# Optimization experiments

Hardware: AMD Instinct MI355X
Metric: run time of the kernel (lower is better)

The kernel has to match this reference:

```python
import jax, jax.numpy as jnp
import numpy as np

B, C, N, M = 4, 192, 160, 160
HEADS, DH = 4, 32
HID = HEADS * DH
NMEM = 4
SCALE = DH ** -0.5


def setup_inputs() -> dict:
    key = jax.random.key(0)
    ks = jax.random.split(key, 8)
    std = 0.05
    return {
        "x": jax.random.normal(ks[0], (B, C, N, M), jnp.float32),
        "gq": jnp.ones((C,), jnp.float32),
        "gk": jnp.ones((C,), jnp.float32),
        "gv": jnp.ones((C,), jnp.float32),
        "Wq": jax.random.normal(ks[1], (HID, C), jnp.float32) * std,
        "Wk": jax.random.normal(ks[2], (HID, C), jnp.float32) * std,
        "Wv": jax.random.normal(ks[3], (HID, C), jnp.float32) * std,
        "mem_kv": jax.random.normal(ks[4], (2, HEADS, NMEM, DH), jnp.float32),
        "Wo": jax.random.normal(ks[5], (C, HID), jnp.float32) * std,
        "bo": jnp.zeros((C,), jnp.float32),
        "Wr": jax.random.normal(ks[6], (C, 2 * C), jnp.float32) * std,
    }


def _rms(x, g):
    # lucidrains RMSNorm over channel axis 1: F.normalize(x, dim=1) * g * sqrt(dim)
    n = jnp.sqrt(jnp.sum(x * x, axis=1, keepdims=True))
    gshape = (1, -1) + (1,) * (x.ndim - 2)
    return x / jnp.maximum(n, 1e-12) * g.reshape(gshape) * jnp.sqrt(jnp.asarray(x.shape[1], x.dtype))


def _axial_attn(q_ft, k_ft, v_map, rep, Wq, Wk, Wv, mem_kv, Wo, bo, gq, gk, gv):
    # q_ft: (b, c, Lq) compact queries (spatial (1,Lq) in the original)
    # k_ft: (b, c, Lk) compact keys; original repeats them `rep` times -> (Lk*rep) keys
    # v_map: (b, c, Lk, rep) values (full map, not broadcast)
    # Exact math of softmax over [NMEM + Lk*rep] keys, exploiting the rep-fold
    # duplicated key scores so attn(key i, copy j) has identical weight p_i:
    #   out = sum_mem p_j mem_v_j + sum_i p_i * (sum_rep v[i, r])
    b = q_ft.shape[0]
    q = jnp.einsum('hdc,bcq->bhqd', Wq.reshape(HEADS, DH, -1), _rms(q_ft, gq))
    k = jnp.einsum('hdc,bck->bhkd', Wk.reshape(HEADS, DH, -1), _rms(k_ft, gk))
    v = jnp.einsum('hdc,bckr->bhkrd', Wv.reshape(HEADS, DH, -1), _rms(v_map, gv))
    v_sum = v.sum(axis=3)  # (b,h,Lk,d)
    mem_k, mem_v = mem_kv[0], mem_kv[1]
    s_k = jnp.einsum('bhqd,bhkd->bhqk', q, k) * SCALE      # (b,h,Lq,Lk)
    s_m = jnp.einsum('bhqd,hjd->bhqj', q, mem_k) * SCALE   # (b,h,Lq,NMEM)
    mx = jnp.maximum(s_k.max(-1), s_m.max(-1))             # (b,h,Lq)
    e_k = jnp.exp(s_k - mx[..., None])
    e_m = jnp.exp(s_m - mx[..., None])
    Z = e_m.sum(-1) + rep * e_k.sum(-1)                    # rep copies of each key
    out = (jnp.einsum('bhqj,hjd->bhqd', e_m, mem_v)
           + jnp.einsum('bhqk,bhkd->bhqd', e_k, v_sum)) / Z[..., None]
    out = out.transpose(0, 2, 1, 3).reshape(b, -1, HID)    # (b,Lq,hid), (h d) channel order
    return jnp.einsum('ck,bqk->bcq', Wo, out) + bo[None, :, None]  # (b,c,Lq)


def reference(x, gq, gk, gv, Wq, Wk, Wv, mem_kv, Wo, bo, Wr):
    # x: (b,c,n,m); mask=None path
    row_ft = x.mean(axis=3)  # (b,c,n)
    col_ft = x.mean(axis=2)  # (b,c,m)
    # row attention: n queries, keys = col_ft repeated n times, values = x^T (spatial (m,n))
    row_attn = _axial_attn(row_ft, col_ft, x.transpose(0, 1, 3, 2), N,
                           Wq, Wk, Wv, mem_kv, Wo, bo, gq, gk, gv)  # (b,c,n)
    # col attention (shared weights): m queries, keys = row_ft repeated m times, values = x
    col_attn = _axial_attn(col_ft, row_ft, x, M,
                           Wq, Wk, Wv, mem_kv, Wo, bo, gq, gk, gv)  # (b,c,m)
    # broadcast to (b,c,n,m), concat on channels, 1x1 conv reduce (bias=False)
    Wr1, Wr2 = Wr[:, :C], Wr[:, C:]
    out = (jnp.einsum('dc,bcn->bdn', Wr1, row_attn)[:, :, :, None]
           + jnp.einsum('dc,bcm->bdm', Wr2, col_attn)[:, :, None, :])
    return out
```

## Files before the change

### kernel.cpp

```cpp
#include <hip/hip_runtime.h>
#include <math.h>

constexpr int B_ = 4, C_ = 192, N_ = 160, M_ = 160;
constexpr int NM_ = N_ * M_;
constexpr float SQRT_C = 13.856406460551018f;
constexpr float SCALE_ = 0.17677669529663687f;

__device__ __forceinline__ float wred_sum(float v) {
    #pragma unroll
    for (int o = 32; o > 0; o >>= 1) v += __shfl_xor(v, o, 64);
    return v;
}
__device__ __forceinline__ float wred_max(float v) {
    #pragma unroll
    for (int o = 32; o > 0; o >>= 1) v = fmaxf(v, __shfl_xor(v, o, 64));
    return v;
}

__global__ __launch_bounds__(256) void prep_rn_kernel(
        const float* __restrict__ x,
        const float* __restrict__ Wr, const float* __restrict__ Wo,
        const float* __restrict__ bo,
        const float* __restrict__ Wq, const float* __restrict__ Wk,
        const float* __restrict__ Wv, const float* __restrict__ gq,
        const float* __restrict__ gk, const float* __restrict__ gv,
        float* __restrict__ rn, float* __restrict__ WfT2,
        float* __restrict__ bfb, float* __restrict__ WT) {
    int bx = blockIdx.x, tid = threadIdx.x;
    if (bx < 400) {
        int g = bx * 256 + tid;
        int b = g / NM_, nm = g - b * NM_;
        const float* xp = x + (size_t)b * (C_ * NM_) + nm;
        float s = 0.f;
        #pragma unroll 16
        for (int c = 0; c < C_; c++) { float v = xp[(size_t)c * NM_]; s += v * v; }
        rn[g] = SQRT_C / fmaxf(sqrtf(s), 1e-12f);
    } else if (bx < 592) {
        int pair = (bx - 400) * 2 + (tid >> 7);
        int hd = tid & 127;
        int t = pair / 192, dch = pair % 192;
        const float* wr = Wr + dch * 384 + t * 192;
        float acc = 0.f;
        for (int c = 0; c < 192; c++) acc += wr[c] * Wo[c * 128 + hd];
        WfT2[pair * 128 + hd] = acc;
        if (hd == 0) {
            float sb = 0.f;
            for (int c = 0; c < 192; c++) sb += wr[c] * bo[c];
            bfb[pair] = sb;
        }
    } else {
        int g = (bx - 592) * 256 + tid;
        int mat = g / 24576, r2 = g - mat * 24576;
        const float* W  = (mat == 0) ? Wq : ((mat == 1) ? Wk : Wv);
        const float* gp = (mat == 0) ? gq : ((mat == 1) ? gk : gv);
        WT[g] = gp[r2 % 192] * W[r2];
    }
}

__global__ __launch_bounds__(512) void rowcol_kernel(
        const float* __restrict__ x, const float* __restrict__ rn,
        float* __restrict__ rowft, float* __restrict__ colft,
        float* __restrict__ Srow, float* __restrict__ Scol) {
    __shared__ float cpart[8][2][160];
    int bc = blockIdx.x;
    int b = bc / C_;
    int tid = threadIdx.x, w = tid >> 6, lane = tid & 63;
    const float* xp = x + (size_t)bc * NM_;
    const float* rp = rn + (size_t)b * NM_;
    int m0 = lane, m1 = lane + 64, m2 = lane + 128;
    bool ok2 = (m2 < M_);
    float cr0 = 0, cr1 = 0, cr2 = 0, cn0 = 0, cn1 = 0, cn2 = 0;
    for (int n = w; n < N_; n += 8) {
        const float* xr = xp + n * M_;
        const float* rr = rp + n * M_;
        float a0 = xr[m0], a1 = xr[m1], a2 = ok2 ? xr[m2] : 0.f;
        float r0 = rr[m0], r1 = rr[m1], r2 = ok2 ? rr[m2] : 0.f;
        float b0 = a0 * r0, b1 = a1 * r1, b2 = a2 * r2;
        cr0 += a0; cr1 += a1; cr2 += a2;
        cn0 += b0; cn1 += b1; cn2 += b2;
        float rs = wred_sum(a0 + a1 + a2);
        float rsn = wred_sum(b0 + b1 + b2);
        if (lane == 0) {
            rowft[bc * N_ + n] = rs * (1.0f / 160.0f);
            Srow[bc * N_ + n] = rsn;
        }
    }
    cpart[w][0][m0] = cr0; cpart[w][0][m1] = cr1; if (ok2) cpart[w][0][m2] = cr2;
    cpart[w][1][m0] = cn0; cpart[w][1][m1] = cn1; if (ok2) cpart[w][1][m2] = cn2;
    __syncthreads();
    if (tid < M_) {
        float sr = 0.f, sn = 0.f;
        #pragma unroll
        for (int ww = 0; ww < 8; ww++) { sr += cpart[ww][0][tid]; sn += cpart[ww][1][tid]; }
        colft[bc * M_ + tid] = sr * (1.0f / 160.0f);
        Scol[bc * M_ + tid] = sn;
    }
}

__global__ __launch_bounds__(256) void proj_kernel(
        const float* __restrict__ WT,
        const float* __restrict__ rowft, const float* __restrict__ colft,
        const float* __restrict__ Srow, const float* __restrict__ Scol,
        float* __restrict__ Qb, float* __restrict__ Kb, float* __restrict__ Vb) {
    __shared__ float in_s[4 * 196];
    __shared__ float sc_s[4];
    int bx = blockIdx.x;
    int pt = bx % 40, rest = bx / 40;
    int mat = rest % 3; int r2 = rest / 3;
    int t = r2 % 2, b = r2 / 2;
    const float* src; float* dst;
    if (mat == 0)      { src = (t == 0) ? rowft : colft; dst = Qb; }
    else if (mat == 1) { src = (t == 0) ? colft : rowft; dst = Kb; }
    else               { src = (t == 0) ? Scol  : Srow;  dst = Vb; }
    const float* Wt = WT + mat * 24576;
    int tid = threadIdx.x;
    for (int idx = tid; idx < 768; idx += 256) {
        int c = idx >> 2, p = idx & 3;
        in_s[p * 196 + c] = src[(b * C_ + c) * 160 + pt * 4 + p];
    }
    __syncthreads();
    int w = tid >> 6, lane = tid & 63;
    if (mat < 2) {
        float v0 = in_s[w * 196 + lane];
        float v1 = in_s[w * 196 + lane + 64];
        float v2 = in_s[w * 196 + lane + 128];
        float ssq = wred_sum(v0 * v0 + v1 * v1 + v2 * v2);
        if (lane == 0) sc_s[w] = SQRT_C / fmaxf(sqrtf(ssq), 1e-12f);
    } else {
        if (tid < 4) sc_s[tid] = 1.0f;
    }
    __syncthreads();
    int hd = tid & 127, p0 = (tid >> 7) * 2;
    const float* wp = Wt + hd * 192;
    const float* i0p = &in_s[p0 * 196];
    const float* i1p = &in_s[(p0 + 1) * 196];
    float a0 = 0.f, a1 = 0.f;
    #pragma unroll 4
    for (int c0 = 0; c0 < 192; c0 += 4) {
        float4 wv = *reinterpret_cast<const float4*>(wp + c0);
        float4 u0 = *reinterpret_cast<const float4*>(i0p + c0);
        float4 u1 = *reinterpret_cast<const float4*>(i1p + c0);
        a0 += wv.x * u0.x + wv.y * u0.y + wv.z * u0.z + wv.w * u0.w;
        a1 += wv.x * u1.x + wv.y * u1.y + wv.z * u1.z + wv.w * u1.w;
    }
    int posbase = (b * 2 + t) * 160 + pt * 4 + p0;
    dst[(size_t)posbase * 128 + hd]       = a0 * sc_s[p0];
    dst[(size_t)(posbase + 1) * 128 + hd] = a1 * sc_s[p0 + 1];
}

__global__ __launch_bounds__(256) void attn_kernel(
        const float* __restrict__ Qb, const float* __restrict__ Kb,
        const float* __restrict__ Vb, const float* __restrict__ memkv,
        float* __restrict__ AO) {
    __shared__ float k_s[160 * 36];
    __shared__ float v_s[32 * 172];
    __shared__ float q_s[8 * 36];
    __shared__ float e_s[8 * 160];
    __shared__ float mk[128];
    __shared__ float mv[128];
    int bx = blockIdx.x;
    int qt = bx % 20; int r = bx / 20;
    int h = r & 3; r >>= 2;
    int t = r & 1; int b = r >> 1;
    int tid = threadIdx.x, w = tid >> 6, lane = tid & 63;
    int btbase = ((b * 2 + t) * 160) * 128 + h * 32;
    for (int idx = tid; idx < 1280; idx += 256) {
        int k = idx >> 3, dq = idx & 7;
        float4 kv = *reinterpret_cast<const float4*>(Kb + btbase + k * 128 + dq * 4);
        *reinterpret_cast<float4*>(&k_s[k * 36 + dq * 4]) = kv;
        float4 vv = *reinterpret_cast<const float4*>(Vb + btbase + k * 128 + dq * 4);
        v_s[(dq * 4 + 0) * 172 + k] = vv.x;
        v_s[(dq * 4 + 1) * 172 + k] = vv.y;
        v_s[(dq * 4 + 2) * 172 + k] = vv.z;
        v_s[(dq * 4 + 3) * 172 + k] = vv.w;
    }
    if (tid < 64) {
        int q = tid >> 3, dq = tid & 7;
        *reinterpret_cast<float4*>(&q_s[q * 36 + dq * 4]) =
            *reinterpret_cast<const float4*>(Qb + btbase + (qt * 8 + q) * 128 + dq * 4);
    }
    if (tid < 128) {
        mk[tid] = memkv[h * 128 + tid];
        mv[tid] = memkv[512 + h * 128 + tid];
    }
    __syncthreads();
    float4 kr0[8], kr1[8], kr2[8];
    #pragma unroll
    for (int dq = 0; dq < 8; dq++) {
        kr0[dq] = *reinterpret_cast<const float4*>(&k_s[lane * 36 + dq * 4]);
        kr1[dq] = *reinterpret_cast<const float4*>(&k_s[(lane + 64) * 36 + dq * 4]);
        if (lane < 32) kr2[dq] = *reinterpret_cast<const float4*>(&k_s[(lane + 128) * 36 + dq * 4]);
        else           kr2[dq] = make_float4(0.f, 0.f, 0.f, 0.f);
    }
    float p;
    {
        int pj = lane >> 3, qi = pj >> 2, j = pj & 3;
        int db = (lane & 7) * 4;
        float4 qv = *reinterpret_cast<const float4*>(&q_s[(w * 2 + qi) * 36 + db]);
        float4 mkv = *reinterpret_cast<const float4*>(&mk[j * 32 + db]);
        p = qv.x * mkv.x + qv.y * mkv.y + qv.z * mkv.z + qv.w * mkv.w;
        p += __shfl_xor(p, 1, 64); p += __shfl_xor(p, 2, 64); p += __shfl_xor(p, 4, 64);
        p *= SCALE_;
    }
    float sm[2][4];
    #pragma unroll
    for (int j = 0; j < 4; j++) {
        sm[0][j] = __shfl(p, j * 8, 64);
        sm[1][j] = __shfl(p, 32 + j * 8, 64);
    }
    int dpv = lane & 31;
    float Zq[2], accm[2];
    #pragma unroll
    for (int qi = 0; qi < 2; qi++) {
        const float* qrow = &q_s[(w * 2 + qi) * 36];
        float s0 = 0.f, s1 = 0.f, s2 = 0.f;
        #pragma unroll
        for (int dq = 0; dq < 8; dq++) {
            float4 qv = *reinterpret_cast<const float4*>(qrow + dq * 4);
            s0 += qv.x * kr0[dq].x + qv.y * kr0[dq].y + qv.z * kr0[dq].z + qv.w * kr0[dq].w;
            s1 += qv.x * kr1[dq].x + qv.y * kr1[dq].y + qv.z * kr1[dq].z + qv.w * kr1[dq].w;
            s2 += qv.x * kr2[dq].x + qv.y * kr2[dq].y + qv.z * kr2[dq].z + qv.w * kr2[dq].w;
        }
        s0 *= SCALE_; s1 *= SCALE_;
        s2 = (lane < 32) ? s2 * SCALE_ : -1e30f;
        float mx = fmaxf(fmaxf(s0, s1), s2);
        mx = fmaxf(mx, fmaxf(fmaxf(sm[qi][0], sm[qi][1]), fmaxf(sm[qi][2], sm[qi][3])));
        mx = wred_max(mx);
        float e0 = __expf(s0 - mx), e1 = __expf(s1 - mx);
        float e2 = (lane < 32) ? __expf(s2 - mx) : 0.f;
        int eb = (w * 2 + qi) * 160;
        e_s[eb + lane] = e0; e_s[eb + 64 + lane] = e1;
        if (lane < 32) e_s[eb + 128 + lane] = e2;
        float esum = wred_sum(e0 + e1 + e2);
        float em0 = __expf(sm[qi][0] - mx), em1 = __expf(sm[qi][1] - mx);
        float em2 = __expf(sm[qi][2] - mx), em3 = __expf(sm[qi][3] - mx);
        Zq[qi] = (em0 + em1 + em2 + em3) + 160.0f * esum;
        accm[qi] = em0 * mv[dpv] + em1 * mv[32 + dpv] + em2 * mv[64 + dpv] + em3 * mv[96 + dpv];
    }
    int half = lane >> 5, k0 = half * 80;
    const float* vrow = &v_s[dpv * 172 + k0];
    const float* e0p = &e_s[(w * 2) * 160 + k0];
    const float* e1p = &e_s[(w * 2 + 1) * 160 + k0];
    float a0 = 0.f, a1 = 0.f;
    #pragma unroll 4
    for (int kk = 0; kk < 80; kk += 4) {
        float4 vv = *reinterpret_cast<const float4*>(vrow + kk);
        float4 e0 = *reinterpret_cast<const float4*>(e0p + kk);
        float4 e1 = *reinterpret_cast<const float4*>(e1p + kk);
        a0 += e0.x * vv.x + e0.y * vv.y + e0.z * vv.z + e0.w * vv.w;
        a1 += e1.x * vv.x + e1.y * vv.y + e1.z * vv.z + e1.w * vv.w;
    }
    a0 += __shfl_down(a0, 32, 64);
    a1 += __shfl_down(a1, 32, 64);
    if (lane < 32) {
        AO[btbase + (qt * 8 + w * 2 + 0) * 128 + lane] = (accm[0] + a0) / Zq[0];
        AO[btbase + (qt * 8 + w * 2 + 1) * 128 + lane] = (accm[1] + a1) / Zq[1];
    }
}

__global__ __launch_bounds__(192) void oproj_kernel(
        const float* __restrict__ WfT2, const float* __restrict__ bfb,
        const float* __restrict__ AO, float* __restrict__ Rr,
        float* __restrict__ Ccv) {
    __shared__ float ao_s[2 * 128];
    int bx = blockIdx.x;
    int pt = bx % 80, rest = bx / 80;
    int t = rest & 1, b = rest >> 1;
    int tid = threadIdx.x;
    for (int idx = tid; idx < 256; idx += 192)
        ao_s[idx] = AO[(size_t)((b * 2 + t) * 160 + pt * 2 + (idx >> 7)) * 128 + (idx & 127)];
    __syncthreads();
    int tofs = t * 192 + tid;
    const float* wp = WfT2 + tofs * 128;
    float a0 = 0.f, a1 = 0.f;
    #pragma unroll 8
    for (int hd = 0; hd < 128; hd += 4) {
        float4 w4 = *reinterpret_cast<const float4*>(wp + hd);
        float4 x0 = *reinterpret_cast<const float4*>(&ao_s[hd]);
        float4 x1 = *reinterpret_cast<const float4*>(&ao_s[128 + hd]);
        a0 += w4.x * x0.x + w4.y * x0.y + w4.z * x0.z + w4.w * x0.w;
        a1 += w4.x * x1.x + w4.y * x1.y + w4.z * x1.z + w4.w * x1.w;
    }
    float bb = bfb[tofs];
    float* dst = t ? Ccv : Rr;
    dst[(b * C_ + tid) * 160 + pt * 2 + 0] = a0 + bb;
    dst[(b * C_ + tid) * 160 + pt * 2 + 1] = a1 + bb;
}

__global__ __launch_bounds__(256) void final_kernel(
        const float* __restrict__ Rr, const float* __restrict__ Ccv,
        float* __restrict__ out) {
    __shared__ float Rl[160];
    __shared__ float Cl[160];
    int bd = blockIdx.x;
    int tid = threadIdx.x;
    if (tid < 160) { Rl[tid] = Rr[bd * 160 + tid]; Cl[tid] = Ccv[bd * 160 + tid]; }
    __syncthreads();
    float* base = out + (size_t)bd * NM_;
    for (int idx = tid; idx < 160 * 40; idx += 256) {
        int n = idx / 40, m4 = idx - n * 40;
        float r = Rl[n];
        float4 v;
        v.x = r + Cl[m4 * 4 + 0];
        v.y = r + Cl[m4 * 4 + 1];
        v.z = r + Cl[m4 * 4 + 2];
        v.w = r + Cl[m4 * 4 + 3];
        *reinterpret_cast<float4*>(base + n * 160 + m4 * 4) = v;
    }
}

extern "C" void kernel_launch(void* const* d_in, const int* in_sizes, int n_in,
                              void* d_out, int out_size, void* d_ws, size_t ws_size,
                              hipStream_t stream) {
    const float* x    = (const float*)d_in[0];
    const float* gq   = (const float*)d_in[1];
    const float* gk   = (const float*)d_in[2];
    const float* gv   = (const float*)d_in[3];
    const float* Wq   = (const float*)d_in[4];
    const float* Wk   = (const float*)d_in[5];
    const float* Wv   = (const float*)d_in[6];
    const float* mkv  = (const float*)d_in[7];
    const float* Wo   = (const float*)d_in[8];
    const float* bo   = (const float*)d_in[9];
    const float* Wr   = (const float*)d_in[10];
    float* out = (float*)d_out;

    float* ws = (float*)d_ws;
    float* rn    = ws;
    float* rowft = rn    + 102400;
    float* colft = rowft + 122880;
    float* Srow  = colft + 122880;
    float* Scol  = Srow  + 122880;
    float* WT    = Scol  + 122880;
    float* Qb    = WT    + 73728;
    float* Kb    = Qb    + 163840;
    float* Vb    = Kb    + 163840;
    float* AO    = Vb    + 163840;
    float* Rr    = AO    + 163840;
    float* Ccv   = Rr    + 122880;
    float* WfT   = Ccv   + 122880;
    float* bfb   = WfT   + 49152;

    prep_rn_kernel<<<880, 256, 0, stream>>>(x, Wr, Wo, bo, Wq, Wk, Wv, gq, gk, gv,
                                            rn, WfT, bfb, WT);
    rowcol_kernel<<<768, 512, 0, stream>>>(x, rn, rowft, colft, Srow, Scol);
    proj_kernel<<<960, 256, 0, stream>>>(WT, rowft, colft, Srow, Scol, Qb, Kb, Vb);
    attn_kernel<<<640, 256, 0, stream>>>(Qb, Kb, Vb, mkv, AO);
    oproj_kernel<<<640, 192, 0, stream>>>(WfT, bfb, AO, Rr, Ccv);
    final_kernel<<<768, 256, 0, stream>>>(Rr, Ccv, out);
}
```

Baseline: 226.6 us.

## Split channel sum-of-squares into chunks and co-schedule row/col means with weight prep

The per-pixel RMS norm reduction over 192 channels is split into 6 chunks of 32 channels, each run by its own block, with partial sums written to a scratch buffer. A new small kernel combines the partials into the reciprocal norm. The unweighted row and column means are moved into the same first launch as the weight preparation, so they run alongside the norm partials. The old fused row/col kernel now computes only the norm-weighted sums. The aim is more blocks in flight to hide load latency in the reduction. The cost is an extra kernel launch, one more full pass over x, and scratch traffic, which reuses the Qb region.

```diff
diff --git a/kernel.cpp b/kernel.cpp
--- a/kernel.cpp
+++ b/kernel.cpp
@@ -17,26 +17,52 @@
     return v;
 }
 
-__global__ __launch_bounds__(256) void prep_rn_kernel(
+__global__ __launch_bounds__(256) void mega1_kernel(
         const float* __restrict__ x,
         const float* __restrict__ Wr, const float* __restrict__ Wo,
         const float* __restrict__ bo,
         const float* __restrict__ Wq, const float* __restrict__ Wk,
         const float* __restrict__ Wv, const float* __restrict__ gq,
         const float* __restrict__ gk, const float* __restrict__ gv,
-        float* __restrict__ rn, float* __restrict__ WfT2,
-        float* __restrict__ bfb, float* __restrict__ WT) {
+        float* __restrict__ psum,
+        float* __restrict__ rowft, float* __restrict__ colft,
+        float* __restrict__ WfT2, float* __restrict__ bfb,
+        float* __restrict__ WT) {
+    __shared__ float cpart[4][160];
     int bx = blockIdx.x, tid = threadIdx.x;
-    if (bx < 400) {
-        int g = bx * 256 + tid;
+    if (bx < 2400) {
+        int chunk = bx / 400, blk = bx % 400;
+        int g = blk * 256 + tid;
         int b = g / NM_, nm = g - b * NM_;
-        const float* xp = x + (size_t)b * (C_ * NM_) + nm;
-        float s = 0.f;
-        #pragma unroll 16
-        for (int c = 0; c < C_; c++) { float v = xp[(size_t)c * NM_]; s += v * v; }
-        rn[g] = SQRT_C / fmaxf(sqrtf(s), 1e-12f);
-    } else if (bx < 592) {
-        int pair = (bx - 400) * 2 + (tid >> 7);
+        const float* xp = x + ((size_t)(b * C_ + chunk * 32)) * NM_ + nm;
+        float ssq = 0.f;
+        #pragma unroll
+        for (int cc = 0; cc < 32; cc++) { float v = xp[(size_t)cc * NM_]; ssq += v * v; }
+        psum[chunk * (B_ * NM_) + g] = ssq;
+    } else if (bx < 3168) {
+        int bc = bx - 2400;
+        int w = tid >> 6, lane = tid & 63;
+        const float* xp = x + (size_t)bc * NM_;
+        int m0 = lane, m1 = lane + 64, m2 = lane + 128;
+        bool ok2 = (m2 < M_);
+        float cr0 = 0.f, cr1 = 0.f, cr2 = 0.f;
+        for (int n = w; n < N_; n += 4) {
+            const float* xr = xp + n * M_;
+            float a0 = xr[m0], a1 = xr[m1], a2 = ok2 ? xr[m2] : 0.f;
+            cr0 += a0; cr1 += a1; cr2 += a2;
+            float rs = wred_sum(a0 + a1 + a2);
+            if (lane == 0) rowft[bc * N_ + n] = rs * (1.0f / 160.0f);
+        }
+        cpart[w][m0] = cr0; cpart[w][m1] = cr1; if (ok2) cpart[w][m2] = cr2;
+        __syncthreads();
+        if (tid < M_) {
+            float sr = 0.f;
+            #pragma unroll
+            for (int ww = 0; ww < 4; ww++) sr += cpart[ww][tid];
+            colft[bc * M_ + tid] = sr * (1.0f / 160.0f);
+        }
+    } else if (bx < 3360) {
+        int pair = (bx - 3168) * 2 + (tid >> 7);
         int hd = tid & 127;
         int t = pair / 192, dch = pair % 192;
         const float* wr = Wr + dch * 384 + t * 192;
@@ -49,7 +75,7 @@
             bfb[pair] = sb;
         }
     } else {
-        int g = (bx - 592) * 256 + tid;
+        int g = (bx - 3360) * 256 + tid;
         int mat = g / 24576, r2 = g - mat * 24576;
         const float* W  = (mat == 0) ? Wq : ((mat == 1) ? Wk : Wv);
         const float* gp = (mat == 0) ? gq : ((mat == 1) ? gk : gv);
@@ -57,11 +83,19 @@
     }
 }
 
-__global__ __launch_bounds__(512) void rowcol_kernel(
+__global__ __launch_bounds__(256) void rnorm_kernel(
+        const float* __restrict__ psum, float* __restrict__ rn) {
+    int g = blockIdx.x * 256 + threadIdx.x;
+    float s = 0.f;
+    #pragma unroll
+    for (int ch = 0; ch < 6; ch++) s += psum[ch * (B_ * NM_) + g];
+    rn[g] = SQRT_C / fmaxf(sqrtf(s), 1e-12f);
+}
+
+__global__ __launch_bounds__(512) void sweighted_kernel(
         const float* __restrict__ x, const float* __restrict__ rn,
-        float* __restrict__ rowft, float* __restrict__ colft,
         float* __restrict__ Srow, float* __restrict__ Scol) {
-    __shared__ float cpart[8][2][160];
+    __shared__ float cpart[8][160];
     int bc = blockIdx.x;
     int b = bc / C_;
     int tid = threadIdx.x, w = tid >> 6, lane = tid & 63;
@@ -69,30 +103,23 @@
     const float* rp = rn + (size_t)b * NM_;
     int m0 = lane, m1 = lane + 64, m2 = lane + 128;
     bool ok2 = (m2 < M_);
-    float cr0 = 0, cr1 = 0, cr2 = 0, cn0 = 0, cn1 = 0, cn2 = 0;
+    float cn0 = 0.f, cn1 = 0.f, cn2 = 0.f;
     for (int n = w; n < N_; n += 8) {
         const float* xr = xp + n * M_;
         const float* rr = rp + n * M_;
-        float a0 = xr[m0], a1 = xr[m1], a2 = ok2 ? xr[m2] : 0.f;
-        float r0 = rr[m0], r1 = rr[m1], r2 = ok2 ? rr[m2] : 0.f;
-        float b0 = a0 * r0, b1 = a1 * r1, b2 = a2 * r2;
-        cr0 += a0; cr1 += a1; cr2 += a2;
+        float b0 = xr[m0] * rr[m0];
+        float b1 = xr[m1] * rr[m1];
+        float b2 = ok2 ? xr[m2] * rr[m2] : 0.f;
         cn0 += b0; cn1 += b1; cn2 += b2;
-        float rs = wred_sum(a0 + a1 + a2);
         float rsn = wred_sum(b0 + b1 + b2);
-        if (lane == 0) {
-            rowft[bc * N_ + n] = rs * (1.0f / 160.0f);
-            Srow[bc * N_ + n] = rsn;
-        }
-    }
-    cpart[w][0][m0] = cr0; cpart[w][0][m1] = cr1; if (ok2) cpart[w][0][m2] = cr2;
-    cpart[w][1][m0] = cn0; cpart[w][1][m1] = cn1; if (ok2) cpart[w][1][m2] = cn2;
+        if (lane == 0) Srow[bc * N_ + n] = rsn;
+    }
+    cpart[w][m0] = cn0; cpart[w][m1] = cn1; if (ok2) cpart[w][m2] = cn2;
     __syncthreads();
     if (tid < M_) {
-        float sr = 0.f, sn = 0.f;
+        float sn = 0.f;
         #pragma unroll
-        for (int ww = 0; ww < 8; ww++) { sr += cpart[ww][0][tid]; sn += cpart[ww][1][tid]; }
-        colft[bc * M_ + tid] = sr * (1.0f / 160.0f);
+        for (int ww = 0; ww < 8; ww++) sn += cpart[ww][tid];
         Scol[bc * M_ + tid] = sn;
     }
 }
@@ -340,10 +367,12 @@
     float* Ccv   = Rr    + 122880;
     float* WfT   = Ccv   + 122880;
     float* bfb   = WfT   + 49152;
-
-    prep_rn_kernel<<<880, 256, 0, stream>>>(x, Wr, Wo, bo, Wq, Wk, Wv, gq, gk, gv,
-                                            rn, WfT, bfb, WT);
-    rowcol_kernel<<<768, 512, 0, stream>>>(x, rn, rowft, colft, Srow, Scol);
+    float* psum  = Qb;
+
+    mega1_kernel<<<3648, 256, 0, stream>>>(x, Wr, Wo, bo, Wq, Wk, Wv, gq, gk, gv,
+                                           psum, rowft, colft, WfT, bfb, WT);
+    rnorm_kernel<<<400, 256, 0, stream>>>(psum, rn);
+    sweighted_kernel<<<768, 512, 0, stream>>>(x, rn, Srow, Scol);
     proj_kernel<<<960, 256, 0, stream>>>(WT, rowft, colft, Srow, Scol, Qb, Kb, Vb);
     attn_kernel<<<640, 256, 0, stream>>>(Qb, Kb, Vb, mkv, AO);
     oproj_kernel<<<640, 192, 0, stream>>>(WfT, bfb, AO, Rr, Ccv);
```

Result: slower. 242.7 us (+7.1%).
